# Optimization experiments

Hardware: AMD Instinct MI355X
Metric: run time of the kernel (lower is better)

The kernel has to match this reference:

```python
import jax, jax.numpy as jnp
import numpy as np

TAU = 2.0
EPS = 1e-5
SG_ALPHA = 4.0  # spikingjelly default Sigmoid surrogate alpha


@jax.custom_vjp
def heaviside(x):
    return (x >= 0.0).astype(x.dtype)

def _heaviside_fwd(x):
    return heaviside(x), x

def _heaviside_bwd(x, g):
    s = jax.nn.sigmoid(SG_ALPHA * x)
    return (g * SG_ALPHA * s * (1.0 - s),)

heaviside.defvjp(_heaviside_fwd, _heaviside_bwd)


def lif(x_seq, v_th):
    """Multi-step LIF, hard reset to 0, detach_reset=True. x_seq: (T, ...)."""
    def step(v, x_t):
        v = v + (x_t - v) / TAU
        s = heaviside(v - v_th)
        v = v * (1.0 - jax.lax.stop_gradient(s))  # detached hard reset
        return v, s
    _, spikes = jax.lax.scan(step, jnp.zeros_like(x_seq[0]), x_seq)
    return spikes


def bn(y, gamma, beta, mean, var):
    # y: (T, B, C, N); inference-mode BatchNorm1d over channel dim
    inv = gamma / jnp.sqrt(var + EPS)
    return y * inv[None, None, :, None] + (beta - mean * inv)[None, None, :, None]


def setup_inputs() -> dict:
    key = jax.random.key(0)
    ks = jax.random.split(key, 8)
    T, B, C, H, W = 4, 32, 256, 32, 32
    d = {
        "x": jax.random.normal(ks[0], (T, B, C, H, W), jnp.float32),
        "q_w": jax.random.normal(ks[1], (C, C), jnp.float32) * (1.0 / np.sqrt(C)),
        "q_gamma": jnp.ones((C,), jnp.float32),
        "q_beta": jnp.zeros((C,), jnp.float32),
        "q_mean": jnp.zeros((C,), jnp.float32),
        "q_var": jnp.ones((C,), jnp.float32),
        "k_w": jax.random.normal(ks[2], (C, C), jnp.float32) * (1.0 / np.sqrt(C)),
        "k_gamma": jnp.ones((C,), jnp.float32),
        "k_beta": jnp.zeros((C,), jnp.float32),
        "k_mean": jnp.zeros((C,), jnp.float32),
        "k_var": jnp.ones((C,), jnp.float32),
        "p_w": jax.random.normal(ks[3], (C, C), jnp.float32) * (1.0 / np.sqrt(C)),
        "p_b": jnp.zeros((C,), jnp.float32),
        "p_gamma": jnp.ones((C,), jnp.float32),
        "p_beta": jnp.zeros((C,), jnp.float32),
        "p_mean": jnp.zeros((C,), jnp.float32),
        "p_var": jnp.ones((C,), jnp.float32),
    }
    return d


def reference(x, q_w, q_gamma, q_beta, q_mean, q_var,
              k_w, k_gamma, k_beta, k_mean, k_var,
              p_w, p_b, p_gamma, p_beta, p_mean, p_var):
    T, B, C, H, W = x.shape
    num_heads = 8
    dh = C // num_heads
    N = H * W
    xs = x.reshape(T, B, C, N)

    # Q branch: 1x1 conv (C x C matmul) -> BN -> LIF
    q = bn(jnp.einsum('oc,tbcn->tbon', q_w, xs), q_gamma, q_beta, q_mean, q_var)
    q_spikes = lif(q, 1.0)                                # (T,B,C,N)
    q_h = q_spikes.reshape(T, B, num_heads, dh, N)

    # K branch
    k = bn(jnp.einsum('oc,tbcn->tbon', k_w, xs), k_gamma, k_beta, k_mean, k_var)
    k_spikes = lif(k, 1.0)
    k_h = k_spikes.reshape(T, B, num_heads, dh, N)

    # channel-sum pooled Q per head -> attn LIF (v_th=0.5) -> elementwise mult with K
    q_sum = jnp.sum(q_h, axis=3, keepdims=True)           # (T,B,h,1,N)
    attn = lif(q_sum, 0.5)
    x_one = attn * k_h                                    # (T,B,h,dh,N)

    # projection: 1x1 conv with bias -> BN -> LIF
    xo = x_one.reshape(T, B, C, N)
    xo = jnp.einsum('oc,tbcn->tbon', p_w, xo) + p_b[None, None, :, None]
    xo = bn(xo, p_gamma, p_beta, p_mean, p_var).reshape(T, B, C, H, W)
    x_final = lif(xo, 1.0)
    return x_final
```

## Files before the change

### kernel.cpp

```cpp
#include <hip/hip_runtime.h>
#include <cstdint>
#include <cstddef>

#define T_DIM 4
#define B_DIM 32
#define C_DIM 256
#define N_DIM 1024
#define NHEAD 8
#define DHEAD 32
#define NWRD 32

__device__ __forceinline__ float lif_step(float& v, float x, float vth) {
    v = __fadd_rn(v, __fmul_rn(__fsub_rn(x, v), 0.5f));
    const float s = (v >= vth) ? 1.0f : 0.0f;
    if (s != 0.0f) v = 0.0f;
    return s;
}

__device__ __forceinline__ void async_copy16(const float* g, float* l) {
    __builtin_amdgcn_global_load_lds(
        (const __attribute__((address_space(1))) unsigned int*)g,
        (__attribute__((address_space(3))) unsigned int*)l, 16, 0, 0);
}

#define FMA_ROW4(r, av)                               \
    acc[(r)*4+0] = fmaf(av, b0.x, acc[(r)*4+0]);      \
    acc[(r)*4+1] = fmaf(av, b0.y, acc[(r)*4+1]);      \
    acc[(r)*4+2] = fmaf(av, b0.z, acc[(r)*4+2]);      \
    acc[(r)*4+3] = fmaf(av, b0.w, acc[(r)*4+3]);

#define FMA_8x4()        \
    FMA_ROW4(0, a0.x)    \
    FMA_ROW4(1, a0.y)    \
    FMA_ROW4(2, a0.z)    \
    FMA_ROW4(3, a0.w)    \
    FMA_ROW4(4, a1.x)    \
    FMA_ROW4(5, a1.y)    \
    FMA_ROW4(6, a1.z)    \
    FMA_ROW4(7, a1.w)

__global__ __launch_bounds__(256) void k_transpose(
    const float* __restrict__ qw, const float* __restrict__ kw,
    const float* __restrict__ pw, float* __restrict__ wqk_t,
    float* __restrict__ p_t)
{
    const int i = blockIdx.x * 256 + threadIdx.x;
    if (i < C_DIM * 512) {
        const int k = i >> 9, col = i & 511;
        const int h = col >> 6, j = col & 63;
        wqk_t[i] = (j < 32) ? qw[(size_t)(h * 32 + j) * C_DIM + k]
                            : kw[(size_t)(h * 32 + j - 32) * C_DIM + k];
    } else {
        const int i2 = i - C_DIM * 512;
        const int k = i2 >> 8, c = i2 & 255;
        p_t[i2] = pw[(size_t)c * C_DIM + k];
    }
}

__global__ __launch_bounds__(512, 4) void k_qk(
    const float* __restrict__ x, const float* __restrict__ wqk,
    const float* __restrict__ qg, const float* __restrict__ qbeta,
    const float* __restrict__ qmean, const float* __restrict__ qvar,
    const float* __restrict__ kg, const float* __restrict__ kbeta,
    const float* __restrict__ kmean, const float* __restrict__ kvar,
    uint32_t* __restrict__ xbits)
{
    __shared__ float w_lds[2][32 * 128];
    __shared__ float x_lds[2][32 * 128];
    __shared__ float inv_lds[128];
    __shared__ float bias_lds[128];
    __shared__ float    qsum_lds[256];
    __shared__ float    attn_lds[256];
    __shared__ uint32_t pack_lds[256];

    const int tid = threadIdx.x;
    const int hp = blockIdx.x, nt = blockIdx.y, b = blockIdx.z;
    const int n0g = nt * 128;

    const int  mg   = tid >> 5;
    const int  m0   = mg << 3;
    const int  ng   = tid & 31;
    const int  n0   = ng << 2;
    const int  hsel = mg >> 3;
    const bool is_q = ((mg & 7) < 4);

    if (tid < 128) {
        const int m = tid;
        const int hs = m >> 6, j = m & 63;
        const int h = hp * 2 + hs;
        const bool q = (j < 32);
        const float* g  = q ? qg    : kg;
        const float* be = q ? qbeta : kbeta;
        const float* me = q ? qmean : kmean;
        const float* va = q ? qvar  : kvar;
        const int ch = h * DHEAD + (q ? j : j - 32);
        const float iv = __fdiv_rn(g[ch], __fsqrt_rn(__fadd_rn(va[ch], 1e-5f)));
        inv_lds[m]  = iv;
        bias_lds[m] = __fsub_rn(be[ch], __fmul_rn(me[ch], iv));
    }

    const int skl  = tid >> 5;
    const int scol = (tid & 31) << 2;
    const float* wgp = wqk + (size_t)skl * 512 + hp * 128 + scol;

    float vstate[32];
    #pragma unroll
    for (int i = 0; i < 32; i++) vstate[i] = 0.0f;
    float v_attn = 0.0f;

    {
        const float* xgp = x + ((size_t)b * C_DIM + skl) * N_DIM + n0g + scol;
        #pragma unroll
        for (int r = 0; r < 2; r++) {
            async_copy16(wgp + (size_t)(r * 16) * 512,  &w_lds[0][r * 2048 + tid * 4]);
            async_copy16(xgp + (size_t)(r * 16) * N_DIM, &x_lds[0][r * 2048 + tid * 4]);
        }
    }

    float acc[32];
    #pragma unroll
    for (int i = 0; i < 32; i++) acc[i] = 0.0f;

    for (int g = 0; g < 32; ++g) {
        const int cur = g & 1;
        __syncthreads();
        if (g + 1 < 32) {
            const int g1 = g + 1, tt = g1 >> 3, kk = (g1 & 7) * 32;
            const float* xgp = x + ((size_t)(tt * B_DIM + b) * C_DIM + kk + skl) * N_DIM
                               + n0g + scol;
            float* wd = &w_lds[1 - cur][0];
            float* xd = &x_lds[1 - cur][0];
            #pragma unroll
            for (int r = 0; r < 2; r++) {
                async_copy16(wgp + (size_t)(kk + r * 16) * 512,  wd + r * 2048 + tid * 4);
                async_copy16(xgp + (size_t)(r * 16) * N_DIM,     xd + r * 2048 + tid * 4);
            }
        }
        {
            const float* wl = &w_lds[cur][0];
            const float* xl = &x_lds[cur][0];
            #pragma unroll 2
            for (int k = 0; k < 32; k++) {
                const float4 a0 = *(const float4*)(wl + k * 128 + m0);
                const float4 a1 = *(const float4*)(wl + k * 128 + m0 + 4);
                const float4 b0 = *(const float4*)(xl + k * 128 + n0);
                FMA_8x4()
            }
        }

        if ((g & 7) == 7) {
            const int t = g >> 3;
            #pragma unroll
            for (int r = 0; r < 8; r++) {
                const float iv = inv_lds[m0 + r];
                const float bs = bias_lds[m0 + r];
                #pragma unroll
                for (int j = 0; j < 4; j++) {
                    const float y = __fadd_rn(__fmul_rn(acc[r * 4 + j], iv), bs);
                    acc[r * 4 + j] = lif_step(vstate[r * 4 + j], y, 1.0f);
                }
            }
            if (tid < 256) { qsum_lds[tid] = 0.0f; pack_lds[tid] = 0u; }
            __syncthreads();
            if (is_q) {
                #pragma unroll
                for (int j = 0; j < 4; j++) {
                    const int col = n0 + j;
                    float cs = acc[j];
                    #pragma unroll
                    for (int r = 1; r < 8; r++) cs += acc[r * 4 + j];
                    atomicAdd(&qsum_lds[hsel * 128 + col], cs);
                }
            }
            __syncthreads();
            if (tid < 256) attn_lds[tid] = lif_step(v_attn, qsum_lds[tid], 0.5f);
            __syncthreads();
            if (!is_q) {
                #pragma unroll
                for (int r = 0; r < 8; r++) {
                    const int krow = ((mg & 7) - 4) * 8 + r;
                    uint32_t nib = 0;
                    #pragma unroll
                    for (int jj = 0; jj < 4; jj++) {
                        if (acc[r * 4 + jj] != 0.0f &&
                            attn_lds[hsel * 128 + n0 + jj] != 0.0f)
                            nib |= (1u << jj);
                    }
                    if (nib) {
                        const int word = ng >> 3;
                        const int shf  = (ng & 7) * 4;
                        atomicOr(&pack_lds[hsel * 128 + krow * 4 + word], nib << shf);
                    }
                }
            }
            __syncthreads();
            if (tid < 256) {
                const int hs2  = tid >> 7;
                const int rem  = tid & 127;
                const int krow = rem >> 2, word = rem & 3;
                const int ch = (hp * 2 + hs2) * DHEAD + krow;
                xbits[((size_t)(t * B_DIM + b) * C_DIM + ch) * NWRD + nt * 4 + word]
                    = pack_lds[tid];
            }
            #pragma unroll
            for (int i = 0; i < 32; i++) acc[i] = 0.0f;
        }
    }
}

__global__ __launch_bounds__(512, 4) void k_proj(
    const uint32_t* __restrict__ xbits, const float* __restrict__ pt,
    const float* __restrict__ pbias, const float* __restrict__ pg,
    const float* __restrict__ pbeta, const float* __restrict__ pmean,
    const float* __restrict__ pvar, float* __restrict__ out)
{
    __shared__ float w_lds[2][32 * 128];
    __shared__ float x_lds[2][32 * 128];
    __shared__ float inv_lds[128];
    __shared__ float bias_lds[128];
    __shared__ float pb_lds[128];

    const int tid = threadIdx.x;
    const int mt = blockIdx.x, nt = blockIdx.y, b = blockIdx.z;
    const int n0g = nt * 128;
    const int c0  = mt * 128;

    const int mg = tid >> 5, m0 = mg << 3;
    const int ng = tid & 31, n0 = ng << 2;

    if (tid < 128) {
        const int ch = c0 + tid;
        const float iv = __fdiv_rn(pg[ch], __fsqrt_rn(__fadd_rn(pvar[ch], 1e-5f)));
        inv_lds[tid]  = iv;
        bias_lds[tid] = __fsub_rn(pbeta[ch], __fmul_rn(pmean[ch], iv));
        pb_lds[tid]   = pbias[ch];
    }

    const int skl  = tid >> 5;
    const int scol = (tid & 31) << 2;
    const float* wgp = pt + (size_t)skl * 256 + c0 + scol;

    const int urow = tid >> 4, cg = tid & 15;
    const int wsel = nt * 4 + (cg >> 2);
    const int ushf = (cg & 3) * 8;

    float vstate[32];
    #pragma unroll
    for (int i = 0; i < 32; i++) vstate[i] = 0.0f;

    #define BITS_AT(G) xbits[((size_t)((G) >> 3) * B_DIM + b) * C_DIM * NWRD \
                             + (size_t)(((G) & 7) * 32 + urow) * NWRD + wsel]

    {
        const uint32_t u0 = BITS_AT(0);
        const uint32_t bits = (u0 >> ushf) & 0xffu;
        float* xw = &x_lds[0][urow * 128 + cg * 8];
        float4 f0, f1;
        f0.x = ((bits >> 0) & 1u) ? 1.0f : 0.0f;
        f0.y = ((bits >> 1) & 1u) ? 1.0f : 0.0f;
        f0.z = ((bits >> 2) & 1u) ? 1.0f : 0.0f;
        f0.w = ((bits >> 3) & 1u) ? 1.0f : 0.0f;
        f1.x = ((bits >> 4) & 1u) ? 1.0f : 0.0f;
        f1.y = ((bits >> 5) & 1u) ? 1.0f : 0.0f;
        f1.z = ((bits >> 6) & 1u) ? 1.0f : 0.0f;
        f1.w = ((bits >> 7) & 1u) ? 1.0f : 0.0f;
        *(float4*)(xw)     = f0;
        *(float4*)(xw + 4) = f1;
        #pragma unroll
        for (int r = 0; r < 2; r++)
            async_copy16(wgp + (size_t)(r * 16) * 256, &w_lds[0][r * 2048 + tid * 4]);
    }
    uint32_t u_a = BITS_AT(1);

    float acc[32];
    #pragma unroll
    for (int i = 0; i < 32; i++) acc[i] = 0.0f;

    for (int g = 0; g < 32; ++g) {
        const int cur = g & 1;
        __syncthreads();
        if (g + 1 < 32) {
            const int kk = ((g + 1) & 7) * 32;
            const uint32_t bits = (u_a >> ushf) & 0xffu;
            float* xw = &x_lds[1 - cur][urow * 128 + cg * 8];
            float4 f0, f1;
            f0.x = ((bits >> 0) & 1u) ? 1.0f : 0.0f;
            f0.y = ((bits >> 1) & 1u) ? 1.0f : 0.0f;
            f0.z = ((bits >> 2) & 1u) ? 1.0f : 0.0f;
            f0.w = ((bits >> 3) & 1u) ? 1.0f : 0.0f;
            f1.x = ((bits >> 4) & 1u) ? 1.0f : 0.0f;
            f1.y = ((bits >> 5) & 1u) ? 1.0f : 0.0f;
            f1.z = ((bits >> 6) & 1u) ? 1.0f : 0.0f;
            f1.w = ((bits >> 7) & 1u) ? 1.0f : 0.0f;
            *(float4*)(xw)     = f0;
            *(float4*)(xw + 4) = f1;
            float* wd = &w_lds[1 - cur][0];
            #pragma unroll
            for (int r = 0; r < 2; r++)
                async_copy16(wgp + (size_t)(kk + r * 16) * 256, wd + r * 2048 + tid * 4);
        }
        if (g + 2 < 32) u_a = BITS_AT(g + 2);
        {
            const float* wl = &w_lds[cur][0];
            const float* xl = &x_lds[cur][0];
            #pragma unroll 2
            for (int k = 0; k < 32; k++) {
                const float4 a0 = *(const float4*)(wl + k * 128 + m0);
                const float4 a1 = *(const float4*)(wl + k * 128 + m0 + 4);
                const float4 b0 = *(const float4*)(xl + k * 128 + n0);
                FMA_8x4()
            }
        }

        if ((g & 7) == 7) {
            const int t = g >> 3;
            #pragma unroll
            for (int r = 0; r < 8; r++) {
                const int ch = c0 + m0 + r;
                const float iv = inv_lds[m0 + r];
                const float bs = bias_lds[m0 + r];
                const float pb = pb_lds[m0 + r];
                float* ob = out + ((size_t)(t * B_DIM + b) * C_DIM + ch) * N_DIM + n0g;
                float ov[4];
                #pragma unroll
                for (int j = 0; j < 4; j++) {
                    float y = __fadd_rn(acc[r * 4 + j], pb);
                    y = __fadd_rn(__fmul_rn(y, iv), bs);
                    ov[j] = lif_step(vstate[r * 4 + j], y, 1.0f);
                }
                float4 o4;
                o4.x = ov[0]; o4.y = ov[1]; o4.z = ov[2]; o4.w = ov[3];
                *(float4*)(ob + n0) = o4;
            }
            #pragma unroll
            for (int i = 0; i < 32; i++) acc[i] = 0.0f;
        }
    }
    #undef BITS_AT
}

extern "C" void kernel_launch(void* const* d_in, const int* in_sizes, int n_in,
                              void* d_out, int out_size, void* d_ws, size_t ws_size,
                              hipStream_t stream) {
    const float* x    = (const float*)d_in[0];
    const float* q_w  = (const float*)d_in[1];
    const float* q_g  = (const float*)d_in[2];
    const float* q_b  = (const float*)d_in[3];
    const float* q_m  = (const float*)d_in[4];
    const float* q_v  = (const float*)d_in[5];
    const float* k_w  = (const float*)d_in[6];
    const float* k_g  = (const float*)d_in[7];
    const float* k_b  = (const float*)d_in[8];
    const float* k_m  = (const float*)d_in[9];
    const float* k_v  = (const float*)d_in[10];
    const float* p_w  = (const float*)d_in[11];
    const float* p_b  = (const float*)d_in[12];
    const float* p_g  = (const float*)d_in[13];
    const float* p_be = (const float*)d_in[14];
    const float* p_m  = (const float*)d_in[15];
    const float* p_v  = (const float*)d_in[16];

    float*    wqk_t = (float*)d_ws;
    float*    p_t   = (float*)((char*)d_ws + 524288);
    uint32_t* xbits = (uint32_t*)((char*)d_ws + 786432);
    float*    out   = (float*)d_out;

    k_transpose<<<768, 256, 0, stream>>>(q_w, k_w, p_w, wqk_t, p_t);

    dim3 g1(NHEAD / 2, N_DIM / 128, B_DIM);
    k_qk<<<g1, 512, 0, stream>>>(x, wqk_t, q_g, q_b, q_m, q_v,
                                 k_g, k_b, k_m, k_v, xbits);

    dim3 g2(C_DIM / 128, N_DIM / 128, B_DIM);
    k_proj<<<g2, 512, 0, stream>>>(xbits, p_t, p_b, p_g, p_be, p_m, p_v, out);
}
```

Before: 846.9 us.

## Read GEMM weights directly from global memory and reorder grid by head

Both GEMM kernels stop staging weight tiles in double-buffered LDS. Instead each thread loads its 8-wide weight slice with float4 global loads inside the k loop; all lanes of a wavefront share the same address, so these loads are broadcasts served by cache. The launch grid is also reordered so that consecutive blocks share the same weight slice (head pair or output-channel tile), which is meant to keep that slice resident in L2. This saves LDS space and async-copy traffic, but it puts global-load latency directly into the inner FMA loop.

```diff
diff --git a/kernel.cpp b/kernel.cpp
--- a/kernel.cpp
+++ b/kernel.cpp
@@ -65,7 +65,6 @@
     const float* __restrict__ kmean, const float* __restrict__ kvar,
     uint32_t* __restrict__ xbits)
 {
-    __shared__ float w_lds[2][32 * 128];
     __shared__ float x_lds[2][32 * 128];
     __shared__ float inv_lds[128];
     __shared__ float bias_lds[128];
@@ -74,7 +73,7 @@
     __shared__ uint32_t pack_lds[256];
 
     const int tid = threadIdx.x;
-    const int hp = blockIdx.x, nt = blockIdx.y, b = blockIdx.z;
+    const int nt = blockIdx.x, b = blockIdx.y, hp = blockIdx.z;
     const int n0g = nt * 128;
 
     const int  mg   = tid >> 5;
@@ -101,7 +100,6 @@
 
     const int skl  = tid >> 5;
     const int scol = (tid & 31) << 2;
-    const float* wgp = wqk + (size_t)skl * 512 + hp * 128 + scol;
 
     float vstate[32];
     #pragma unroll
@@ -111,10 +109,8 @@
     {
         const float* xgp = x + ((size_t)b * C_DIM + skl) * N_DIM + n0g + scol;
         #pragma unroll
-        for (int r = 0; r < 2; r++) {
-            async_copy16(wgp + (size_t)(r * 16) * 512,  &w_lds[0][r * 2048 + tid * 4]);
+        for (int r = 0; r < 2; r++)
             async_copy16(xgp + (size_t)(r * 16) * N_DIM, &x_lds[0][r * 2048 + tid * 4]);
-        }
     }
 
     float acc[32];
@@ -128,21 +124,18 @@
             const int g1 = g + 1, tt = g1 >> 3, kk = (g1 & 7) * 32;
             const float* xgp = x + ((size_t)(tt * B_DIM + b) * C_DIM + kk + skl) * N_DIM
                                + n0g + scol;
-            float* wd = &w_lds[1 - cur][0];
             float* xd = &x_lds[1 - cur][0];
             #pragma unroll
-            for (int r = 0; r < 2; r++) {
-                async_copy16(wgp + (size_t)(kk + r * 16) * 512,  wd + r * 2048 + tid * 4);
-                async_copy16(xgp + (size_t)(r * 16) * N_DIM,     xd + r * 2048 + tid * 4);
-            }
+            for (int r = 0; r < 2; r++)
+                async_copy16(xgp + (size_t)(r * 16) * N_DIM, xd + r * 2048 + tid * 4);
         }
         {
-            const float* wl = &w_lds[cur][0];
+            const float* wg = wqk + (size_t)((g & 7) * 32) * 512 + hp * 128 + m0;
             const float* xl = &x_lds[cur][0];
             #pragma unroll 2
             for (int k = 0; k < 32; k++) {
-                const float4 a0 = *(const float4*)(wl + k * 128 + m0);
-                const float4 a1 = *(const float4*)(wl + k * 128 + m0 + 4);
+                const float4 a0 = *(const float4*)(wg + (size_t)k * 512);
+                const float4 a1 = *(const float4*)(wg + (size_t)k * 512 + 4);
                 const float4 b0 = *(const float4*)(xl + k * 128 + n0);
                 FMA_8x4()
             }
@@ -214,14 +207,13 @@
     const float* __restrict__ pbeta, const float* __restrict__ pmean,
     const float* __restrict__ pvar, float* __restrict__ out)
 {
-    __shared__ float w_lds[2][32 * 128];
     __shared__ float x_lds[2][32 * 128];
     __shared__ float inv_lds[128];
     __shared__ float bias_lds[128];
     __shared__ float pb_lds[128];
 
     const int tid = threadIdx.x;
-    const int mt = blockIdx.x, nt = blockIdx.y, b = blockIdx.z;
+    const int nt = blockIdx.x, b = blockIdx.y, mt = blockIdx.z;
     const int n0g = nt * 128;
     const int c0  = mt * 128;
 
@@ -235,10 +227,6 @@
         bias_lds[tid] = __fsub_rn(pbeta[ch], __fmul_rn(pmean[ch], iv));
         pb_lds[tid]   = pbias[ch];
     }
-
-    const int skl  = tid >> 5;
-    const int scol = (tid & 31) << 2;
-    const float* wgp = pt + (size_t)skl * 256 + c0 + scol;
 
     const int urow = tid >> 4, cg = tid & 15;
     const int wsel = nt * 4 + (cg >> 2);
@@ -266,9 +254,6 @@
         f1.w = ((bits >> 7) & 1u) ? 1.0f : 0.0f;
         *(float4*)(xw)     = f0;
         *(float4*)(xw + 4) = f1;
-        #pragma unroll
-        for (int r = 0; r < 2; r++)
-            async_copy16(wgp + (size_t)(r * 16) * 256, &w_lds[0][r * 2048 + tid * 4]);
     }
     uint32_t u_a = BITS_AT(1);
 
@@ -280,7 +265,6 @@
         const int cur = g & 1;
         __syncthreads();
         if (g + 1 < 32) {
-            const int kk = ((g + 1) & 7) * 32;
             const uint32_t bits = (u_a >> ushf) & 0xffu;
             float* xw = &x_lds[1 - cur][urow * 128 + cg * 8];
             float4 f0, f1;
@@ -294,19 +278,15 @@
             f1.w = ((bits >> 7) & 1u) ? 1.0f : 0.0f;
             *(float4*)(xw)     = f0;
             *(float4*)(xw + 4) = f1;
-            float* wd = &w_lds[1 - cur][0];
-            #pragma unroll
-            for (int r = 0; r < 2; r++)
-                async_copy16(wgp + (size_t)(kk + r * 16) * 256, wd + r * 2048 + tid * 4);
         }
         if (g + 2 < 32) u_a = BITS_AT(g + 2);
         {
-            const float* wl = &w_lds[cur][0];
+            const float* wg = pt + (size_t)((g & 7) * 32) * 256 + c0 + m0;
             const float* xl = &x_lds[cur][0];
             #pragma unroll 2
             for (int k = 0; k < 32; k++) {
-                const float4 a0 = *(const float4*)(wl + k * 128 + m0);
-                const float4 a1 = *(const float4*)(wl + k * 128 + m0 + 4);
+                const float4 a0 = *(const float4*)(wg + (size_t)k * 256);
+                const float4 a1 = *(const float4*)(wg + (size_t)k * 256 + 4);
                 const float4 b0 = *(const float4*)(xl + k * 128 + n0);
                 FMA_8x4()
             }
@@ -367,10 +347,10 @@
 
     k_transpose<<<768, 256, 0, stream>>>(q_w, k_w, p_w, wqk_t, p_t);
 
-    dim3 g1(NHEAD / 2, N_DIM / 128, B_DIM);
+    dim3 g1(N_DIM / 128, B_DIM, NHEAD / 2);
     k_qk<<<g1, 512, 0, stream>>>(x, wqk_t, q_g, q_b, q_m, q_v,
                                  k_g, k_b, k_m, k_v, xbits);
 
-    dim3 g2(C_DIM / 128, N_DIM / 128, B_DIM);
+    dim3 g2(N_DIM / 128, B_DIM, C_DIM / 128);
     k_proj<<<g2, 512, 0, stream>>>(xbits, p_t, p_b, p_g, p_be, p_m, p_v, out);
 }
```

New measurement: 1.008 ms. 19.0% more time.
